# Kernel optimization log

Hardware: AMD Instinct MI355X
Metric: run time of the kernel (lower is better)

Reference implementation:

```python
import jax, jax.numpy as jnp
import numpy as np

N_NODES = 3070
N_FEAT = 128
N_OUT = 64
H_SIZE = 50
N_EDGES = 49120
BATCH = 128


def setup_inputs() -> dict:
    key = jax.random.key(0)
    ks = jax.random.split(key, 8)
    x_in = jax.random.normal(ks[0], (BATCH, N_NODES, N_FEAT), dtype=jnp.float32)
    edge_index = jax.random.randint(ks[1], (2, N_EDGES), 0, N_NODES, dtype=jnp.int64)
    edge_weight = jax.random.uniform(ks[2], (N_EDGES,), dtype=jnp.float32)
    W = jax.random.normal(ks[3], (N_FEAT, N_OUT), dtype=jnp.float32) / np.sqrt(N_FEAT)
    b = jnp.zeros((N_OUT,), dtype=jnp.float32)
    W_ih = jax.random.normal(ks[4], (H_SIZE, N_OUT), dtype=jnp.float32) / np.sqrt(N_OUT)
    W_hh = jax.random.normal(ks[5], (H_SIZE, H_SIZE), dtype=jnp.float32) / np.sqrt(H_SIZE)
    b_ih = jnp.zeros((H_SIZE,), dtype=jnp.float32)
    b_hh = jnp.zeros((H_SIZE,), dtype=jnp.float32)
    h0 = jax.random.normal(ks[6], (N_NODES, H_SIZE), dtype=jnp.float32)
    return {"x_in": x_in, "edge_index": edge_index, "edge_weight": edge_weight,
            "W": W, "b": b, "W_ih": W_ih, "W_hh": W_hh, "b_ih": b_ih,
            "b_hh": b_hh, "h0": h0}


def _gcn(x, edge_index, edge_weight, W, b):
    # x: (B, N, F). Vectorized GCNConv over the per-sample python loop.
    n = x.shape[1]
    # vectorized form of the dict-based edge-id remap: rank among unique ids
    uniq = jnp.unique(edge_index, size=n, fill_value=2 ** 30)
    ei = jnp.searchsorted(uniq, edge_index)
    src, dst = ei[0], ei[1]
    # GCNConv default: add self loops with weight 1, symmetric normalization
    loop = jnp.arange(n)
    src = jnp.concatenate([src, loop])
    dst = jnp.concatenate([dst, loop])
    ew = jnp.concatenate([edge_weight, jnp.ones((n,), dtype=x.dtype)])
    deg = jax.ops.segment_sum(ew, dst, num_segments=n)
    dinv = jnp.where(deg > 0, jax.lax.rsqrt(deg), jnp.zeros_like(deg))
    norm = dinv[src] * ew * dinv[dst]                 # (E+N,)
    xw = jnp.einsum('bnf,fo->bno', x, W)              # transform first
    msg = xw[:, src, :] * norm[None, :, None]         # (B, E+N, O)
    out = jnp.zeros_like(xw).at[:, dst, :].add(msg)   # scatter-add to targets
    return out + b


def reference(x_in, edge_index, edge_weight, W, b, W_ih, W_hh, b_ih, b_hh, h0):
    # GCN over all B graph samples (shared fixed graph)
    x = _gcn(x_in, edge_index, edge_weight, W, b)     # (B, N, O)
    # input_horizon==3 -> exactly one horizon step; the torch RNN is seq-first,
    # so seq_len = B (sample dim) and batch = N_NODES, hidden hardcoded 50.
    def step(h, xt):                                   # xt: (N, O), h: (N, H)
        h = jnp.tanh(xt @ W_ih.T + b_ih + h @ W_hh.T + b_hh)
        return h, h
    _, x_out = jax.lax.scan(step, h0, x)               # (B, N, H)
    return x_out
```

## Files before the change

### kernel.cpp

```cpp
#include <hip/hip_runtime.h>

#define NN 3070
#define NF 128
#define NO 64
#define NH 50
#define NC 52
#define NE 49120
#define NB 128
#define BCH 32
#define NCHUNK 4
#define MCH (BCH * NN)
#define GCAP 1024


__global__ __launch_bounds__(256) void zero_kernel(int* __restrict__ p, int n) {
  int i = blockIdx.x * 256 + threadIdx.x;
  if (i < n) p[i] = 0;
}

__global__ __launch_bounds__(256) void mark_kernel(const int* __restrict__ ei, int* __restrict__ mark) {
  int i = blockIdx.x * 256 + threadIdx.x;
  if (i < 2 * NE) mark[ei[i]] = 1;
}

__global__ __launch_bounds__(1024) void exscan_kernel(const int* __restrict__ in, int* __restrict__ out,
                                                      int n, int write_total) {
  __shared__ int part[1024];
  int tid = threadIdx.x;
  int base = tid * 3;
  int v0 = (base + 0 < n) ? in[base + 0] : 0;
  int v1 = (base + 1 < n) ? in[base + 1] : 0;
  int v2 = (base + 2 < n) ? in[base + 2] : 0;
  int s = v0 + v1 + v2;
  part[tid] = s;
  __syncthreads();
  for (int off = 1; off < 1024; off <<= 1) {
    int t = (tid >= off) ? part[tid - off] : 0;
    __syncthreads();
    part[tid] += t;
    __syncthreads();
  }
  int run = part[tid] - s;
  if (base + 0 < n) out[base + 0] = run; run += v0;
  if (base + 1 < n) out[base + 1] = run; run += v1;
  if (base + 2 < n) out[base + 2] = run;
  if (write_total && tid == 1023) out[n] = part[1023];
}

__global__ __launch_bounds__(256) void remap_deg_kernel(const int* __restrict__ ei, const float* __restrict__ ew,
    const int* __restrict__ ranks, int* __restrict__ srcr, int* __restrict__ dstr,
    int* __restrict__ degc, float* __restrict__ degw) {
  int e = blockIdx.x * 256 + threadIdx.x;
  if (e >= NE) return;
  int s = ranks[ei[e]];
  int d = ranks[ei[NE + e]];
  srcr[e] = s;
  dstr[e] = d;
  atomicAdd(&degc[d], 1);
  atomicAdd(&degw[d], ew[e]);
}

__global__ __launch_bounds__(256) void dinv_kernel(const float* __restrict__ degw,
    float* __restrict__ dinv, float* __restrict__ selfn) {
  int n = blockIdx.x * 256 + threadIdx.x;
  if (n >= NN) return;
  float dg = degw[n] + 1.0f;
  float di = rsqrtf(dg);
  dinv[n] = di;
  selfn[n] = di * di;
}

__global__ __launch_bounds__(256) void csr_fill_kernel(const float* __restrict__ ew, const int* __restrict__ srcr,
    const int* __restrict__ dstr, const int* __restrict__ rowptr, int* __restrict__ cursor,
    const float* __restrict__ dinv, int* __restrict__ csr_src, float* __restrict__ csr_norm) {
  int e = blockIdx.x * 256 + threadIdx.x;
  if (e >= NE) return;
  int d = dstr[e];
  int s = srcr[e];
  int pos = rowptr[d] + atomicAdd(&cursor[d], 1);
  csr_src[pos] = s;
  csr_norm[pos] = dinv[s] * ew[e] * dinv[d];
}

__global__ __launch_bounds__(256) void wfold_kernel(const float* __restrict__ W,
    const float* __restrict__ Wih, const float* __restrict__ b,
    const float* __restrict__ bih, const float* __restrict__ bhh,
    float* __restrict__ Wp, float* __restrict__ bp) {
  int idx = blockIdx.x * 256 + threadIdx.x;
  if (idx < 128 * 64) {
    int k = idx >> 6, j = idx & 63;
    float s = 0.f;
    if (j < NH) {
      for (int o = 0; o < NO; ++o) s += W[k * NO + o] * Wih[j * NO + o];
    }
    Wp[k * 64 + j] = s;
  }
  if (idx < NC) {
    float s = 0.f;
    if (idx < NH) {
      for (int o = 0; o < NO; ++o) s += b[o] * Wih[idx * NO + o];
      s += bih[idx] + bhh[idx];
    }
    bp[idx] = s;
  }
}

__global__ __launch_bounds__(256) void gemm_kernel(const float* __restrict__ A,
    const float* __restrict__ W, float* __restrict__ out, int M) {
  __shared__ float As[128 * 68];
  __shared__ float Ws[32 * 64];
  int tid = threadIdx.x;
  int row0 = blockIdx.x * 128;
  int rg = tid >> 3;
  int cg = tid & 7;
  int c0 = cg * 8;
  float acc[4][8];
#pragma unroll
  for (int i = 0; i < 4; ++i)
#pragma unroll
    for (int j = 0; j < 8; ++j) acc[i][j] = 0.f;

  for (int kc = 0; kc < 4; ++kc) {
#pragma unroll
    for (int j = 0; j < 4; ++j) {
      int f = tid + 256 * j;
      int r = f >> 3, kq = f & 7;
      int grow = row0 + r;
      float4 v = make_float4(0.f, 0.f, 0.f, 0.f);
      if (grow < M) v = *(const float4*)&A[(size_t)grow * NF + kc * 32 + kq * 4];
      *(float4*)&As[r * 68 + kq * 4] = v;
    }
#pragma unroll
    for (int j = 0; j < 2; ++j) {
      int f = tid + 256 * j;
      int kk = f >> 4, cq = f & 15;
      *(float4*)&Ws[kk * 64 + cq * 4] = *(const float4*)&W[(size_t)(kc * 32 + kk) * 64 + cq * 4];
    }
    __syncthreads();
#pragma unroll 2
    for (int k4 = 0; k4 < 32; k4 += 4) {
      float4 a[4];
#pragma unroll
      for (int i = 0; i < 4; ++i) a[i] = *(const float4*)&As[(rg + 32 * i) * 68 + k4];
#pragma unroll
      for (int m = 0; m < 4; ++m) {
        float4 w0 = *(const float4*)&Ws[(k4 + m) * 64 + c0];
        float4 w1 = *(const float4*)&Ws[(k4 + m) * 64 + c0 + 4];
#pragma unroll
        for (int i = 0; i < 4; ++i) {
          float av = (m == 0) ? a[i].x : (m == 1) ? a[i].y : (m == 2) ? a[i].z : a[i].w;
          acc[i][0] += av * w0.x; acc[i][1] += av * w0.y;
          acc[i][2] += av * w0.z; acc[i][3] += av * w0.w;
          acc[i][4] += av * w1.x; acc[i][5] += av * w1.y;
          acc[i][6] += av * w1.z; acc[i][7] += av * w1.w;
        }
      }
    }
    __syncthreads();
  }
#pragma unroll
  for (int i = 0; i < 4; ++i) {
    int r = row0 + rg + 32 * i;
    if (r < M) {
      if (c0 < NC)
        *(float4*)&out[(size_t)r * NC + c0] = make_float4(acc[i][0], acc[i][1], acc[i][2], acc[i][3]);
      if (c0 + 4 < NC)
        *(float4*)&out[(size_t)r * NC + c0 + 4] = make_float4(acc[i][4], acc[i][5], acc[i][6], acc[i][7]);
    }
  }
}

__global__ __launch_bounds__(256) void gather_kernel(const float4* __restrict__ xw,
    const int* __restrict__ rowptr, const int* __restrict__ csr_src, const float* __restrict__ csr_norm,
    const float* __restrict__ selfn, const float* __restrict__ bp, float4* __restrict__ outg, int b0) {
  __shared__ int s_src[GCAP];
  __shared__ float s_nrm[GCAP];
  int tid = threadIdx.x;
  int f4 = tid & 15, nl = tid >> 4;
  int nb = blockIdx.x * 16;
  int b = blockIdx.y;
  int nend = nb + 16 < NN ? nb + 16 : NN;
  int be0 = rowptr[nb], be1 = rowptr[nend];
  int cnt = be1 - be0;
  int scnt = cnt < GCAP ? cnt : GCAP;
  for (int i = tid; i < scnt; i += 256) {
    s_src[i] = csr_src[be0 + i];
    s_nrm[i] = csr_norm[be0 + i];
  }
  __syncthreads();
  int n = nb + nl;
  if (n >= NN || f4 >= 13) return;
  const float4* xb = xw + (size_t)b * NN * 13;
  float sn = selfn[n];
  float4 v = xb[n * 13 + f4];
  float ax = v.x * sn, ay = v.y * sn, az = v.z * sn, aw = v.w * sn;
  float bx = 0.f, by = 0.f, bz = 0.f, bw = 0.f;
  int le0 = rowptr[n] - be0, le1 = rowptr[n + 1] - be0;
  int lim = le1 < GCAP ? le1 : GCAP;
  int e = le0;
  for (; e + 1 < lim; e += 2) {
    int s1 = s_src[e], s2 = s_src[e + 1];
    float w1 = s_nrm[e], w2 = s_nrm[e + 1];
    float4 u1 = xb[s1 * 13 + f4];
    float4 u2 = xb[s2 * 13 + f4];
    ax += w1 * u1.x; ay += w1 * u1.y; az += w1 * u1.z; aw += w1 * u1.w;
    bx += w2 * u2.x; by += w2 * u2.y; bz += w2 * u2.z; bw += w2 * u2.w;
  }
  if (e < lim) {
    int s1 = s_src[e];
    float w1 = s_nrm[e];
    float4 u1 = xb[s1 * 13 + f4];
    ax += w1 * u1.x; ay += w1 * u1.y; az += w1 * u1.z; aw += w1 * u1.w;
  }
  for (e = (le0 > GCAP ? le0 : GCAP); e < le1; ++e) {
    int s1 = csr_src[be0 + e];
    float w1 = csr_norm[be0 + e];
    float4 u1 = xb[s1 * 13 + f4];
    ax += w1 * u1.x; ay += w1 * u1.y; az += w1 * u1.z; aw += w1 * u1.w;
  }
  float4 bb = ((const float4*)bp)[f4];
  float4 o = make_float4(ax + bx + bb.x, ay + by + bb.y, az + bz + bb.z, aw + bw + bb.w);
  outg[((size_t)(b0 + b) * NN + n) * 13 + f4] = o;
}

__global__ __launch_bounds__(256, 3) void rnn_kernel(const float* __restrict__ pre,
    const float* __restrict__ Whh, const float* __restrict__ h0, float* __restrict__ out) {
  __shared__ float hs[6 * 52];
  int tid = threadIdx.x;
  int n0 = blockIdx.x * 5;
  int nl = tid / 50;
  int j = tid - nl * 50;
  bool active = tid < 250;
  int jj = active ? j : 0;
  float2 whh2[25];
  const float2* whhp = (const float2*)(Whh + jj * NH);
#pragma unroll
  for (int q = 0; q < 25; ++q) whh2[q] = whhp[q];
  if (tid < 6 * 52) hs[tid] = 0.f;
  if (tid + 256 < 6 * 52) hs[tid + 256] = 0.f;
  __syncthreads();
  if (active) hs[nl * 52 + j] = h0[n0 * 50 + tid];
  const size_t NPRE = (size_t)NN * NC;
  const size_t NOUT = (size_t)NN * NH;
  int nn = active ? (n0 + nl) : n0;
  const float* prep = pre + (size_t)nn * NC + jj;
  float xpre = prep[0];
  __syncthreads();
  for (int t = 0; t < NB; ++t) {
    float a0 = xpre, a1 = 0.f, a2 = 0.f, a3 = 0.f;
    if (t + 1 < NB) xpre = prep[(size_t)(t + 1) * NPRE];
    const float4* hr = (const float4*)&hs[nl * 52];
#pragma unroll
    for (int q = 0; q < 12; q += 4) {
      float4 h0v = hr[q], h1v = hr[q + 1], h2v = hr[q + 2], h3v = hr[q + 3];
      a0 += h0v.x * whh2[2*q].x   + h0v.y * whh2[2*q].y   + h0v.z * whh2[2*q+1].x + h0v.w * whh2[2*q+1].y;
      a1 += h1v.x * whh2[2*q+2].x + h1v.y * whh2[2*q+2].y + h1v.z * whh2[2*q+3].x + h1v.w * whh2[2*q+3].y;
      a2 += h2v.x * whh2[2*q+4].x + h2v.y * whh2[2*q+4].y + h2v.z * whh2[2*q+5].x + h2v.w * whh2[2*q+5].y;
      a3 += h3v.x * whh2[2*q+6].x + h3v.y * whh2[2*q+6].y + h3v.z * whh2[2*q+7].x + h3v.w * whh2[2*q+7].y;
    }
    {
      float2 ht = *(const float2*)&hs[nl * 52 + 48];
      a0 += ht.x * whh2[24].x + ht.y * whh2[24].y;
    }
    float v = (a0 + a1) + (a2 + a3);
    float e = __expf(-2.f * fabsf(v));
    float r = (1.f - e) * __builtin_amdgcn_rcpf(1.f + e);
    float hnew = (v < 0.f) ? -r : r;
    __syncthreads();
    if (active) {
      hs[nl * 52 + j] = hnew;
      out[(size_t)t * NOUT + n0 * 50 + tid] = hnew;
    }
    __syncthreads();
  }
}


extern "C" void kernel_launch(void* const* d_in, const int* in_sizes, int n_in,
                              void* d_out, int out_size, void* d_ws, size_t ws_size,
                              hipStream_t stream) {
  const float* x_in = (const float*)d_in[0];
  const int* ei     = (const int*)d_in[1];
  const float* ew   = (const float*)d_in[2];
  const float* W    = (const float*)d_in[3];
  const float* bias = (const float*)d_in[4];
  const float* Wih  = (const float*)d_in[5];
  const float* Whh  = (const float*)d_in[6];
  const float* bih  = (const float*)d_in[7];
  const float* bhh  = (const float*)d_in[8];
  const float* h0   = (const float*)d_in[9];
  float* out = (float*)d_out;

  char* ws = (char*)d_ws;
  size_t off = 0;
  auto alloc = [&](size_t bytes) {
    size_t o = off;
    off += (bytes + 255) & ~(size_t)255;
    return o;
  };
  float* xw    = (float*)(ws + alloc((size_t)MCH * NC * 4));
  float* gcn   = (float*)(ws + alloc((size_t)NB * NN * NC * 4));
  int*   zb    = (int*)(ws + alloc((size_t)4 * NN * 4));
  int* mark = zb;
  int* degc = zb + NN;
  float* degw = (float*)(zb + 2 * NN);
  int* cursor = zb + 3 * NN;
  int*   ranks  = (int*)(ws + alloc(NN * 4));
  int*   srcr   = (int*)(ws + alloc(NE * 4));
  int*   dstr   = (int*)(ws + alloc(NE * 4));
  float* dinv   = (float*)(ws + alloc(NN * 4));
  float* selfn  = (float*)(ws + alloc(NN * 4));
  int*   rowptr = (int*)(ws + alloc((NN + 1) * 4));
  int*   csrc   = (int*)(ws + alloc(NE * 4));
  float* cnorm  = (float*)(ws + alloc(NE * 4));
  float* Wp     = (float*)(ws + alloc(128 * 64 * 4));
  float* bp     = (float*)(ws + alloc(NC * 4));

  zero_kernel<<<(4 * NN + 255) / 256, 256, 0, stream>>>(zb, 4 * NN);
  mark_kernel<<<(2 * NE + 255) / 256, 256, 0, stream>>>(ei, mark);
  exscan_kernel<<<1, 1024, 0, stream>>>(mark, ranks, NN, 0);
  remap_deg_kernel<<<(NE + 255) / 256, 256, 0, stream>>>(ei, ew, ranks, srcr, dstr, degc, degw);
  dinv_kernel<<<(NN + 255) / 256, 256, 0, stream>>>(degw, dinv, selfn);
  exscan_kernel<<<1, 1024, 0, stream>>>(degc, rowptr, NN, 1);
  csr_fill_kernel<<<(NE + 255) / 256, 256, 0, stream>>>(ew, srcr, dstr, rowptr, cursor, dinv, csrc, cnorm);
  wfold_kernel<<<32, 256, 0, stream>>>(W, Wih, bias, bih, bhh, Wp, bp);

  for (int c = 0; c < NCHUNK; ++c) {
    gemm_kernel<<<(MCH + 127) / 128, 256, 0, stream>>>(
        x_in + (size_t)c * MCH * NF, Wp, xw, MCH);
    dim3 gg((NN + 15) / 16, BCH);
    gather_kernel<<<gg, 256, 0, stream>>>(
        (const float4*)xw, rowptr, csrc, cnorm, selfn, bp, (float4*)gcn, c * BCH);
  }
  rnn_kernel<<<(NN + 4) / 5, 256, 0, stream>>>(gcn, Whh, h0, out);
}
```

Before: 618.0 us.

## Process all samples in one GEMM and gather launch with larger row tiles

Drops the four-chunk loop so the projection GEMM and the neighbour gather each run once over all 128 samples. The GEMM tile grows from 128 to 256 rows per block with 8x8 accumulators per thread, a narrower shared-memory row stride, and no row bounds checks (MTOT is divisible by 256). This cuts launch count and improves weight reuse per block, but needs a workspace xw buffer four times larger, so the intermediate can no longer stay cache-resident between GEMM and gather. Register pressure also rises, with an occupancy hint of 3.

```diff
diff --git a/kernel.cpp b/kernel.cpp
--- a/kernel.cpp
+++ b/kernel.cpp
@@ -7,9 +7,7 @@
 #define NC 52
 #define NE 49120
 #define NB 128
-#define BCH 32
-#define NCHUNK 4
-#define MCH (BCH * NN)
+#define MTOT (NB * NN)
 #define GCAP 1024
 
 
@@ -105,30 +103,28 @@
   }
 }
 
-__global__ __launch_bounds__(256) void gemm_kernel(const float* __restrict__ A,
-    const float* __restrict__ W, float* __restrict__ out, int M) {
-  __shared__ float As[128 * 68];
+__global__ __launch_bounds__(256, 3) void gemm_kernel(const float* __restrict__ A,
+    const float* __restrict__ W, float* __restrict__ out) {
+  __shared__ float As[256 * 36];
   __shared__ float Ws[32 * 64];
   int tid = threadIdx.x;
-  int row0 = blockIdx.x * 128;
+  int row0 = blockIdx.x * 256;
   int rg = tid >> 3;
   int cg = tid & 7;
   int c0 = cg * 8;
-  float acc[4][8];
-#pragma unroll
-  for (int i = 0; i < 4; ++i)
+  float acc[8][8];
+#pragma unroll
+  for (int i = 0; i < 8; ++i)
 #pragma unroll
     for (int j = 0; j < 8; ++j) acc[i][j] = 0.f;
 
   for (int kc = 0; kc < 4; ++kc) {
 #pragma unroll
-    for (int j = 0; j < 4; ++j) {
+    for (int j = 0; j < 8; ++j) {
       int f = tid + 256 * j;
       int r = f >> 3, kq = f & 7;
-      int grow = row0 + r;
-      float4 v = make_float4(0.f, 0.f, 0.f, 0.f);
-      if (grow < M) v = *(const float4*)&A[(size_t)grow * NF + kc * 32 + kq * 4];
-      *(float4*)&As[r * 68 + kq * 4] = v;
+      float4 v = *(const float4*)&A[(size_t)(row0 + r) * NF + kc * 32 + kq * 4];
+      *(float4*)&As[r * 36 + kq * 4] = v;
     }
 #pragma unroll
     for (int j = 0; j < 2; ++j) {
@@ -139,15 +135,15 @@
     __syncthreads();
 #pragma unroll 2
     for (int k4 = 0; k4 < 32; k4 += 4) {
-      float4 a[4];
-#pragma unroll
-      for (int i = 0; i < 4; ++i) a[i] = *(const float4*)&As[(rg + 32 * i) * 68 + k4];
+      float4 a[8];
+#pragma unroll
+      for (int i = 0; i < 8; ++i) a[i] = *(const float4*)&As[(rg + 32 * i) * 36 + k4];
 #pragma unroll
       for (int m = 0; m < 4; ++m) {
         float4 w0 = *(const float4*)&Ws[(k4 + m) * 64 + c0];
         float4 w1 = *(const float4*)&Ws[(k4 + m) * 64 + c0 + 4];
 #pragma unroll
-        for (int i = 0; i < 4; ++i) {
+        for (int i = 0; i < 8; ++i) {
           float av = (m == 0) ? a[i].x : (m == 1) ? a[i].y : (m == 2) ? a[i].z : a[i].w;
           acc[i][0] += av * w0.x; acc[i][1] += av * w0.y;
           acc[i][2] += av * w0.z; acc[i][3] += av * w0.w;
@@ -159,20 +155,18 @@
     __syncthreads();
   }
 #pragma unroll
-  for (int i = 0; i < 4; ++i) {
-    int r = row0 + rg + 32 * i;
-    if (r < M) {
-      if (c0 < NC)
-        *(float4*)&out[(size_t)r * NC + c0] = make_float4(acc[i][0], acc[i][1], acc[i][2], acc[i][3]);
-      if (c0 + 4 < NC)
-        *(float4*)&out[(size_t)r * NC + c0 + 4] = make_float4(acc[i][4], acc[i][5], acc[i][6], acc[i][7]);
-    }
+  for (int i = 0; i < 8; ++i) {
+    size_t r = row0 + rg + 32 * i;
+    if (c0 < NC)
+      *(float4*)&out[r * NC + c0] = make_float4(acc[i][0], acc[i][1], acc[i][2], acc[i][3]);
+    if (c0 + 4 < NC)
+      *(float4*)&out[r * NC + c0 + 4] = make_float4(acc[i][4], acc[i][5], acc[i][6], acc[i][7]);
   }
 }
 
 __global__ __launch_bounds__(256) void gather_kernel(const float4* __restrict__ xw,
     const int* __restrict__ rowptr, const int* __restrict__ csr_src, const float* __restrict__ csr_norm,
-    const float* __restrict__ selfn, const float* __restrict__ bp, float4* __restrict__ outg, int b0) {
+    const float* __restrict__ selfn, const float* __restrict__ bp, float4* __restrict__ outg) {
   __shared__ int s_src[GCAP];
   __shared__ float s_nrm[GCAP];
   int tid = threadIdx.x;
@@ -220,7 +214,7 @@
   }
   float4 bb = ((const float4*)bp)[f4];
   float4 o = make_float4(ax + bx + bb.x, ay + by + bb.y, az + bz + bb.z, aw + bw + bb.w);
-  outg[((size_t)(b0 + b) * NN + n) * 13 + f4] = o;
+  outg[((size_t)b * NN + n) * 13 + f4] = o;
 }
 
 __global__ __launch_bounds__(256, 3) void rnn_kernel(const float* __restrict__ pre,
@@ -298,8 +292,8 @@
     off += (bytes + 255) & ~(size_t)255;
     return o;
   };
-  float* xw    = (float*)(ws + alloc((size_t)MCH * NC * 4));
-  float* gcn   = (float*)(ws + alloc((size_t)NB * NN * NC * 4));
+  float* xw    = (float*)(ws + alloc((size_t)MTOT * NC * 4));
+  float* gcn   = (float*)(ws + alloc((size_t)MTOT * NC * 4));
   int*   zb    = (int*)(ws + alloc((size_t)4 * NN * 4));
   int* mark = zb;
   int* degc = zb + NN;
@@ -325,12 +319,9 @@
   csr_fill_kernel<<<(NE + 255) / 256, 256, 0, stream>>>(ew, srcr, dstr, rowptr, cursor, dinv, csrc, cnorm);
   wfold_kernel<<<32, 256, 0, stream>>>(W, Wih, bias, bih, bhh, Wp, bp);
 
-  for (int c = 0; c < NCHUNK; ++c) {
-    gemm_kernel<<<(MCH + 127) / 128, 256, 0, stream>>>(
-        x_in + (size_t)c * MCH * NF, Wp, xw, MCH);
-    dim3 gg((NN + 15) / 16, BCH);
-    gather_kernel<<<gg, 256, 0, stream>>>(
-        (const float4*)xw, rowptr, csrc, cnorm, selfn, bp, (float4*)gcn, c * BCH);
-  }
+  gemm_kernel<<<MTOT / 256, 256, 0, stream>>>(x_in, Wp, xw);
+  dim3 gg((NN + 15) / 16, NB);
+  gather_kernel<<<gg, 256, 0, stream>>>(
+      (const float4*)xw, rowptr, csrc, cnorm, selfn, bp, (float4*)gcn);
   rnn_kernel<<<(NN + 4) / 5, 256, 0, stream>>>(gcn, Whh, h0, out);
 }
```

Result: faster. 575.9 us (-6.8%).
